# Optimization experiments

Measured on AMD Instinct MI355X. Metric: run time of the kernel, lower is better.

The kernel has to match this reference:

```python
import jax, jax.numpy as jnp
import numpy as np

G = 9.8          # gravity constant from the module
B = 1024         # buckets per mid layer == spigots per bucket
M = 14           # number of homogeneous mid layers
L = M + 2        # total network layers (head bucket + mids + outlet layer)


def _solve_bucket(H0, S_b, theta_b, inflow):
    """Faithful port of solve_single_bucket.
    H0: scalar head, S_b: (n_sp, 2) [spigot height, area], theta_b: (n_sp,),
    inflow: scalar. Sequential spigot loop -> lax.scan.
    Note: after the first spigot, H_effective = H0 - cum_q/2 (inflow dropped),
    exactly as in the torch code."""
    def step(carry, x):
        H_eff, cum = carry
        sp_h, sp_a, th = x
        h = jnp.maximum(0.0, H_eff - sp_h)
        q = th * jnp.sqrt(2.0 * G * h) * sp_a
        cum = cum + q
        return (H0 - 0.5 * cum, cum), q
    init = (H0 + inflow, jnp.zeros((), S_b.dtype))
    (_, cum_q), qs = jax.lax.scan(step, init, (S_b[:, 0], S_b[:, 1], theta_b))
    H_final = H0 - cum_q + inflow
    return H_final, qs


def setup_inputs() -> dict:
    key = jax.random.key(0)
    ks = jax.random.split(key, 10)
    H0 = jax.random.uniform(ks[0], (1,), jnp.float32) * 5.0
    H_mid = jax.random.uniform(ks[1], (M, B), jnp.float32) * 5.0
    H_last = jax.random.uniform(ks[2], (B,), jnp.float32) * 5.0
    S0 = jax.random.uniform(ks[3], (1, B, 2), jnp.float32)
    S_mid = jax.random.uniform(ks[4], (M, B, B, 2), jnp.float32)
    S_last = jax.random.uniform(ks[5], (B, 1, 2), jnp.float32)
    theta0 = jax.random.uniform(ks[6], (B,), jnp.float32)
    theta_mid = jax.random.uniform(ks[7], (M, B, B), jnp.float32)
    theta_last = jax.random.uniform(ks[8], (B,), jnp.float32)
    precip = jax.random.uniform(ks[9], (), jnp.float32) * 2.0
    return {"H0": H0, "H_mid": H_mid, "H_last": H_last,
            "S0": S0, "S_mid": S_mid, "S_last": S_last,
            "theta0": theta0, "theta_mid": theta_mid, "theta_last": theta_last,
            "precip": precip}


def reference(H0, H_mid, H_last, S0, S_mid, S_last, theta0, theta_mid, theta_last, precip):
    p_layer = precip / L            # precip_inflow_per_layer ('even')
    p_bucket = p_layer / B          # per-bucket share in B-bucket layers

    # layer 0: single head bucket with B spigots, inflow = precip/L
    H0_new, q0 = _solve_bucket(H0[0], S0[0], theta0, p_layer)
    inflow = q0 + p_bucket          # inflow to each of layer-1's B buckets

    # mid layers: vmap over buckets, scan over layers (sequential dependency)
    def mid_layer(inflow, xs):
        H_l, S_l, th_l = xs         # (B,), (B,B,2), (B,B)
        Hn, q = jax.vmap(_solve_bucket)(H_l, S_l, th_l, inflow)
        return q.sum(axis=0) + p_bucket, Hn
    inflow, H_mid_new = jax.lax.scan(mid_layer, inflow, (H_mid, S_mid, theta_mid))

    # last layer: B buckets with a single outlet spigot each
    H_last_new, q_last = jax.vmap(_solve_bucket)(H_last, S_last, theta_last[:, None], inflow)

    # flat output: new heads of all layers + outlet flows
    return jnp.concatenate([H0_new[None], H_mid_new.reshape(-1), H_last_new, q_last.reshape(-1)])
```

## Files before the change

kernel.cpp:

```cpp
#include <hip/hip_runtime.h>
#include <math.h>

#define TWO_G 19.6f
#define NPART 256

__device__ __forceinline__ float flow_q(float th, float d, float a) {
    return th * sqrtf(TWO_G * d) * a;
}

__device__ __forceinline__ float wave_sum(float v) {
#pragma unroll
    for (int o = 32; o > 0; o >>= 1) v += __shfl_xor(v, o);
    return v;
}

__global__ __launch_bounds__(64)
void layer0_kernel(const float* __restrict__ H0p, const float* __restrict__ S0,
                   const float* __restrict__ theta0, const float* __restrict__ precip,
                   float* __restrict__ out, float* __restrict__ P0)
{
    const int lane = threadIdx.x;
    const float H  = H0p[0];
    const float pl = precip[0] * 0.0625f;

    const float2* S2 = (const float2*)S0;
    float2 sv[16]; float tv[16];
#pragma unroll
    for (int c = 0; c < 16; ++c) { sv[c] = S2[c * 64 + lane]; tv[c] = theta0[c * 64 + lane]; }

    float h0 = __shfl(sv[0].x, 0);
    float a0 = __shfl(sv[0].y, 0);
    float t0 = __shfl(tv[0], 0);
    float d0 = (H + pl) - h0;
    float q0 = (d0 > 0.0f) ? flow_q(t0, d0, a0) : 0.0f;
    float cum = q0;
    float u   = H - 0.5f * cum;
    if (lane == 0) P0[0] = q0;

#pragma unroll
    for (int c = 0; c < 16; ++c) {
        int i = c * 64 + lane;
        float2 s = sv[c];
        unsigned long long avail = (c == 0) ? ~1ull : ~0ull;
        unsigned long long cand  = __ballot(s.x < u) & avail;
        float qmine = 0.0f;
        while (cand) {
            int j = __builtin_ctzll(cand);
            float hj = __shfl(s.x, j);
            float aj = __shfl(s.y, j);
            float tj = __shfl(tv[c], j);
            float d = u - hj;
            float q = flow_q(tj, d, aj);
            cum += q;
            u = H - 0.5f * cum;
            if (lane == j) qmine = q;
            if (j >= 63) break;
            avail &= (~0ull << (j + 1));
            cand = __ballot(s.x < u) & avail;
        }
        if (i > 0) P0[i] = qmine;
    }
    if (lane == 0) out[0] = (H - cum) + pl;
}

__global__ __launch_bounds__(256)
void mid_kernel(const float* __restrict__ Hl, const float* __restrict__ Sl,
                const float* __restrict__ thl, const float* __restrict__ Pin,
                int npart, float* __restrict__ Pout, float* __restrict__ outl,
                const float* __restrict__ precip)
{
    __shared__ float acc[1024];
    const int tid  = threadIdx.x;
    const int lane = tid & 63;
    const int b    = blockIdx.x * 4 + (tid >> 6);

#pragma unroll
    for (int r = 0; r < 4; ++r) acc[r * 256 + tid] = 0.0f;
    __syncthreads();

    const float pb = precip[0] * (0.0625f / 1024.0f);

    float part = 0.0f;
    for (int k = lane; k < npart; k += 64) part += Pin[k * 1024 + b];

    const float2* S2   = (const float2*)Sl + (size_t)b * 1024;
    const float*  thrw = thl + (size_t)b * 1024;
    float2 sv[16]; float tv[16];
#pragma unroll
    for (int c = 0; c < 16; ++c) { sv[c] = S2[c * 64 + lane]; tv[c] = thrw[c * 64 + lane]; }

    const float H      = Hl[b];
    const float inflow = pb + wave_sum(part);

    float h0 = __shfl(sv[0].x, 0);
    float a0 = __shfl(sv[0].y, 0);
    float t0 = __shfl(tv[0], 0);
    float d0 = (H + inflow) - h0;
    float q0 = (d0 > 0.0f) ? flow_q(t0, d0, a0) : 0.0f;
    float cum = q0;
    float u   = H - 0.5f * cum;
    if (lane == 0 && q0 != 0.0f) atomicAdd(&acc[0], q0);

#pragma unroll
    for (int c = 0; c < 16; ++c) {
        float2 s = sv[c];
        unsigned long long avail = (c == 0) ? ~1ull : ~0ull;
        unsigned long long cand  = __ballot(s.x < u) & avail;
        float qmine = 0.0f;
        while (cand) {
            int j = __builtin_ctzll(cand);
            float hj = __shfl(s.x, j);
            float aj = __shfl(s.y, j);
            float tj = __shfl(tv[c], j);
            float d = u - hj;
            float q = flow_q(tj, d, aj);
            cum += q;
            u = H - 0.5f * cum;
            if (lane == j) qmine = q;
            if (j >= 63) break;
            avail &= (~0ull << (j + 1));
            cand = __ballot(s.x < u) & avail;
        }
        if (qmine != 0.0f) atomicAdd(&acc[c * 64 + lane], qmine);
    }
    if (lane == 0) outl[b] = (H - cum) + inflow;

    __syncthreads();
#pragma unroll
    for (int r = 0; r < 4; ++r)
        Pout[(size_t)blockIdx.x * 1024 + r * 256 + tid] = acc[r * 256 + tid];
}

__global__ __launch_bounds__(256)
void last_kernel(const float* __restrict__ Hlast, const float* __restrict__ Slast,
                 const float* __restrict__ thlast, const float* __restrict__ Pin,
                 const float* __restrict__ precip, float* __restrict__ out)
{
    const int lane = threadIdx.x & 63;
    const int b    = blockIdx.x * 4 + (threadIdx.x >> 6);
    const float pb = precip[0] * (0.0625f / 1024.0f);

    float part = 0.0f;
#pragma unroll
    for (int k = 0; k < NPART / 64; ++k) part += Pin[(k * 64 + lane) * 1024 + b];
    float inflow = pb + wave_sum(part);

    if (lane == 0) {
        float H = Hlast[b];
        float2 s = ((const float2*)Slast)[b];
        float d = (H + inflow) - s.x;
        float q = (d > 0.0f) ? flow_q(thlast[b], d, s.y) : 0.0f;
        out[1 + 14 * 1024 + b]        = (H - q) + inflow;
        out[1 + 14 * 1024 + 1024 + b] = q;
    }
}

extern "C" void kernel_launch(void* const* d_in, const int* in_sizes, int n_in,
                              void* d_out, int out_size, void* d_ws, size_t ws_size,
                              hipStream_t stream)
{
    (void)in_sizes; (void)n_in; (void)out_size; (void)ws_size;
    const float* H0     = (const float*)d_in[0];
    const float* Hmid   = (const float*)d_in[1];
    const float* Hlast  = (const float*)d_in[2];
    const float* S0     = (const float*)d_in[3];
    const float* Smid   = (const float*)d_in[4];
    const float* Slast  = (const float*)d_in[5];
    const float* th0    = (const float*)d_in[6];
    const float* thmid  = (const float*)d_in[7];
    const float* thlast = (const float*)d_in[8];
    const float* precip = (const float*)d_in[9];
    float* out = (float*)d_out;
    float* PA  = (float*)d_ws;
    float* PB  = PA + (size_t)NPART * 1024;

    layer0_kernel<<<1, 64, 0, stream>>>(H0, S0, th0, precip, out, PA);

    float* cur = PA;
    float* nxt = PB;
    int npart = 1;
    for (int l = 0; l < 14; ++l) {
        mid_kernel<<<256, 256, 0, stream>>>(Hmid + (size_t)l * 1024,
                                            Smid + (size_t)l * 1024 * 1024 * 2,
                                            thmid + (size_t)l * 1024 * 1024,
                                            cur, npart, nxt,
                                            out + 1 + (size_t)l * 1024,
                                            precip);
        float* t = cur; cur = nxt; nxt = t;
        npart = NPART;
    }

    last_kernel<<<256, 256, 0, stream>>>(Hlast, Slast, thlast, cur, precip, out);
}
```

Baseline: 301.2 us.

## Precompute spigot terms, ballot once per chunk, and coalesce partial-flow layout

Each spigot's head offset and flow coefficient (theta*area*sqrt(2g)) are precomputed per lane, so the sequential scan only needs an fma, a sqrt and a multiply per step. The candidate ballot is now taken once per 64-spigot chunk rather than after every accepted spigot; stale candidates are filtered by a d>0 check, and the next candidate's shuffles are software-pipelined. The partial-flow workspace is transposed so each block's inflow reduction reads contiguous data, and the first barrier is moved after the loads. The cost is that every chunk candidate is visited even after it becomes inactive, which adds serial steps when many spigots are initially submerged.

```diff
diff --git a/kernel.cpp b/kernel.cpp
--- a/kernel.cpp
+++ b/kernel.cpp
@@ -1,17 +1,46 @@
 #include <hip/hip_runtime.h>
 #include <math.h>
 
-#define TWO_G 19.6f
-#define NPART 256
-
-__device__ __forceinline__ float flow_q(float th, float d, float a) {
-    return th * sqrtf(TWO_G * d) * a;
-}
+#define SQ2G 4.42718872424f
 
 __device__ __forceinline__ float wave_sum(float v) {
 #pragma unroll
     for (int o = 32; o > 0; o >>= 1) v += __shfl_xor(v, o);
     return v;
+}
+
+template<int FIRST_AVAIL>
+__device__ __forceinline__ void drain(const float* e, const float* cc, int lane,
+                                      float& cum, float* qmine)
+{
+#pragma unroll
+    for (int c = 0; c < 16; ++c) {
+        float hc = 0.5f * cum;
+        unsigned long long cand = __ballot(e[c] > hc);
+        if (c == 0 && FIRST_AVAIL) cand &= ~1ull;
+        float qm = 0.0f;
+        if (cand) {
+            int j = __builtin_ctzll(cand); cand &= cand - 1;
+            float ej = __shfl(e[c], j);
+            float cj = __shfl(cc[c], j);
+            while (true) {
+                bool more = (cand != 0);
+                int jn = 0; float en = 0.0f, cn = 0.0f;
+                if (more) {
+                    jn = __builtin_ctzll(cand); cand &= cand - 1;
+                    en = __shfl(e[c], jn);
+                    cn = __shfl(cc[c], jn);
+                }
+                float d = fmaf(-0.5f, cum, ej);
+                float q = (d > 0.0f) ? cj * sqrtf(d) : 0.0f;
+                cum += q;
+                if (lane == j) qm = q;
+                if (!more) break;
+                j = jn; ej = en; cj = cn;
+            }
+        }
+        qmine[c] = qm;
+    }
 }
 
 __global__ __launch_bounds__(64)
@@ -24,41 +53,28 @@
     const float pl = precip[0] * 0.0625f;
 
     const float2* S2 = (const float2*)S0;
-    float2 sv[16]; float tv[16];
-#pragma unroll
-    for (int c = 0; c < 16; ++c) { sv[c] = S2[c * 64 + lane]; tv[c] = theta0[c * 64 + lane]; }
-
-    float h0 = __shfl(sv[0].x, 0);
-    float a0 = __shfl(sv[0].y, 0);
-    float t0 = __shfl(tv[0], 0);
-    float d0 = (H + pl) - h0;
-    float q0 = (d0 > 0.0f) ? flow_q(t0, d0, a0) : 0.0f;
+    float e[16], cc[16];
+#pragma unroll
+    for (int c = 0; c < 16; ++c) {
+        float2 s = S2[c * 64 + lane];
+        float t  = theta0[c * 64 + lane];
+        e[c]  = H - s.x;
+        cc[c] = t * s.y * SQ2G;
+    }
+
+    float e0 = __shfl(e[0], 0), c0 = __shfl(cc[0], 0);
+    float d0 = e0 + pl;
+    float q0 = (d0 > 0.0f) ? c0 * sqrtf(d0) : 0.0f;
     float cum = q0;
-    float u   = H - 0.5f * cum;
-    if (lane == 0) P0[0] = q0;
+
+    float qmine[16];
+    drain<1>(e, cc, lane, cum, qmine);
 
 #pragma unroll
     for (int c = 0; c < 16; ++c) {
         int i = c * 64 + lane;
-        float2 s = sv[c];
-        unsigned long long avail = (c == 0) ? ~1ull : ~0ull;
-        unsigned long long cand  = __ballot(s.x < u) & avail;
-        float qmine = 0.0f;
-        while (cand) {
-            int j = __builtin_ctzll(cand);
-            float hj = __shfl(s.x, j);
-            float aj = __shfl(s.y, j);
-            float tj = __shfl(tv[c], j);
-            float d = u - hj;
-            float q = flow_q(tj, d, aj);
-            cum += q;
-            u = H - 0.5f * cum;
-            if (lane == j) qmine = q;
-            if (j >= 63) break;
-            avail &= (~0ull << (j + 1));
-            cand = __ballot(s.x < u) & avail;
-        }
-        if (i > 0) P0[i] = qmine;
+        float q = (i == 0) ? q0 : qmine[c];
+        P0[(i >> 2) * 1024 + (i & 3)] = q;
     }
     if (lane == 0) out[0] = (H - cum) + pl;
 }
@@ -72,63 +88,58 @@
     __shared__ float acc[1024];
     const int tid  = threadIdx.x;
     const int lane = tid & 63;
-    const int b    = blockIdx.x * 4 + (tid >> 6);
+    const int w    = tid >> 6;
+    const int b    = blockIdx.x * 4 + w;
 
 #pragma unroll
     for (int r = 0; r < 4; ++r) acc[r * 256 + tid] = 0.0f;
-    __syncthreads();
 
     const float pb = precip[0] * (0.0625f / 1024.0f);
-
-    float part = 0.0f;
-    for (int k = lane; k < npart; k += 64) part += Pin[k * 1024 + b];
+    const float H  = Hl[b];
 
     const float2* S2   = (const float2*)Sl + (size_t)b * 1024;
     const float*  thrw = thl + (size_t)b * 1024;
-    float2 sv[16]; float tv[16];
-#pragma unroll
-    for (int c = 0; c < 16; ++c) { sv[c] = S2[c * 64 + lane]; tv[c] = thrw[c * 64 + lane]; }
-
-    const float H      = Hl[b];
+    float e[16], cc[16];
+#pragma unroll
+    for (int c = 0; c < 16; ++c) {
+        float2 s = S2[c * 64 + lane];
+        float t  = thrw[c * 64 + lane];
+        e[c]  = H - s.x;
+        cc[c] = t * s.y * SQ2G;
+    }
+
+    float part = 0.0f;
+    const float* prow = Pin + (size_t)blockIdx.x * 1024 + w;
+#pragma unroll
+    for (int k = 0; k < 4; ++k) {
+        int src = k * 64 + lane;
+        if (src < npart) part += prow[src * 4];
+    }
     const float inflow = pb + wave_sum(part);
 
-    float h0 = __shfl(sv[0].x, 0);
-    float a0 = __shfl(sv[0].y, 0);
-    float t0 = __shfl(tv[0], 0);
-    float d0 = (H + inflow) - h0;
-    float q0 = (d0 > 0.0f) ? flow_q(t0, d0, a0) : 0.0f;
+    __syncthreads();
+
+    float e0 = __shfl(e[0], 0), c0 = __shfl(cc[0], 0);
+    float d0 = e0 + inflow;
+    float q0 = (d0 > 0.0f) ? c0 * sqrtf(d0) : 0.0f;
     float cum = q0;
-    float u   = H - 0.5f * cum;
     if (lane == 0 && q0 != 0.0f) atomicAdd(&acc[0], q0);
 
-#pragma unroll
-    for (int c = 0; c < 16; ++c) {
-        float2 s = sv[c];
-        unsigned long long avail = (c == 0) ? ~1ull : ~0ull;
-        unsigned long long cand  = __ballot(s.x < u) & avail;
-        float qmine = 0.0f;
-        while (cand) {
-            int j = __builtin_ctzll(cand);
-            float hj = __shfl(s.x, j);
-            float aj = __shfl(s.y, j);
-            float tj = __shfl(tv[c], j);
-            float d = u - hj;
-            float q = flow_q(tj, d, aj);
-            cum += q;
-            u = H - 0.5f * cum;
-            if (lane == j) qmine = q;
-            if (j >= 63) break;
-            avail &= (~0ull << (j + 1));
-            cand = __ballot(s.x < u) & avail;
-        }
-        if (qmine != 0.0f) atomicAdd(&acc[c * 64 + lane], qmine);
-    }
+    float qmine[16];
+    drain<1>(e, cc, lane, cum, qmine);
+
+#pragma unroll
+    for (int c = 0; c < 16; ++c)
+        if (qmine[c] != 0.0f) atomicAdd(&acc[c * 64 + lane], qmine[c]);
+
     if (lane == 0) outl[b] = (H - cum) + inflow;
 
     __syncthreads();
 #pragma unroll
-    for (int r = 0; r < 4; ++r)
-        Pout[(size_t)blockIdx.x * 1024 + r * 256 + tid] = acc[r * 256 + tid];
+    for (int r = 0; r < 4; ++r) {
+        int i = r * 256 + tid;
+        Pout[(i >> 2) * 1024 + blockIdx.x * 4 + (i & 3)] = acc[i];
+    }
 }
 
 __global__ __launch_bounds__(256)
@@ -137,19 +148,21 @@
                  const float* __restrict__ precip, float* __restrict__ out)
 {
     const int lane = threadIdx.x & 63;
-    const int b    = blockIdx.x * 4 + (threadIdx.x >> 6);
+    const int w    = threadIdx.x >> 6;
+    const int b    = blockIdx.x * 4 + w;
     const float pb = precip[0] * (0.0625f / 1024.0f);
 
     float part = 0.0f;
-#pragma unroll
-    for (int k = 0; k < NPART / 64; ++k) part += Pin[(k * 64 + lane) * 1024 + b];
+    const float* prow = Pin + (size_t)blockIdx.x * 1024 + w;
+#pragma unroll
+    for (int k = 0; k < 4; ++k) part += prow[(k * 64 + lane) * 4];
     float inflow = pb + wave_sum(part);
 
     if (lane == 0) {
         float H = Hlast[b];
         float2 s = ((const float2*)Slast)[b];
         float d = (H + inflow) - s.x;
-        float q = (d > 0.0f) ? flow_q(thlast[b], d, s.y) : 0.0f;
+        float q = (d > 0.0f) ? thlast[b] * sqrtf(19.6f * d) * s.y : 0.0f;
         out[1 + 14 * 1024 + b]        = (H - q) + inflow;
         out[1 + 14 * 1024 + 1024 + b] = q;
     }
@@ -172,7 +185,7 @@
     const float* precip = (const float*)d_in[9];
     float* out = (float*)d_out;
     float* PA  = (float*)d_ws;
-    float* PB  = PA + (size_t)NPART * 1024;
+    float* PB  = PA + (size_t)256 * 1024;
 
     layer0_kernel<<<1, 64, 0, stream>>>(H0, S0, th0, precip, out, PA);
 
@@ -187,7 +200,7 @@
                                             out + 1 + (size_t)l * 1024,
                                             precip);
         float* t = cur; cur = nxt; nxt = t;
-        npart = NPART;
+        npart = 256;
     }
 
     last_kernel<<<256, 256, 0, stream>>>(Hlast, Slast, thlast, cur, precip, out);
```

After: 422.5 us. +40.3%, slower.
